# Performance work log

Measured on AMD Instinct MI355X. Metric: run time of the kernel, lower is better.

## Reference

```python
import jax, jax.numpy as jnp
import numpy as np

B, S, D = 32, 256, 384
MAX_LEN = 4096
DUR_MAX = 16  # durations in [0, 16)


def setup_inputs() -> dict:
    key = jax.random.key(0)
    kx, kd = jax.random.split(key)
    x = jax.random.normal(kx, (B, S, D), dtype=jnp.float32)
    duration = jax.random.randint(kd, (B, S), 0, DUR_MAX, dtype=jnp.int64)
    return {"x": x, "duration": duration, "max_len": MAX_LEN}


def reference(x, duration, max_len):
    # Length regulation: repeat row i of x[b] duration[b, i] times, then pad
    # each batch element with zeros to max_len frames.
    # Equivalent vectorized form: frame t of batch b copies phoneme index
    #   idx = searchsorted(cumsum(duration[b]), t, side='right')
    # and frames beyond total duration are zero.
    Bx, Sx, Dx = x.shape
    cum = jnp.cumsum(duration, axis=1)          # [B, S] cumulative frame ends
    mel_len = cum[:, -1]                        # [B] total frames per batch
    t = jnp.arange(max_len)                     # [T]
    # For each batch row, map each output frame t -> source phoneme index.
    idx = jax.vmap(lambda c: jnp.searchsorted(c, t, side='right'))(cum)  # [B, T]
    idx = jnp.clip(idx, 0, Sx - 1)
    out = jnp.take_along_axis(x, idx[:, :, None], axis=1)  # [B, T, D] gather
    mask = (t[None, :] < mel_len[:, None])                  # [B, T] valid frames
    out = out * mask[:, :, None].astype(x.dtype)            # zero-pad tail
    return out, mel_len
```

## Files before the change

kernel.cpp:

```cpp
#include <hip/hip_runtime.h>


constexpr int B  = 32;
constexpr int S  = 256;
constexpr int D  = 384;
constexpr int ML = 4096;
constexpr int D4 = D / 4;
constexpr int ROWS = 16;
constexpr int TB = 256;

__global__ __launch_bounds__(TB) void lr_scan_kernel(const int* __restrict__ dur,
                                                     int* __restrict__ cum,
                                                     float* __restrict__ mel_out) {
    const int b = blockIdx.x;
    const int tid = threadIdx.x;
    __shared__ int s[S];
    s[tid] = dur[b * S + tid];
    __syncthreads();
    for (int off = 1; off < S; off <<= 1) {
        int v = (tid >= off) ? s[tid - off] : 0;
        __syncthreads();
        s[tid] += v;
        __syncthreads();
    }
    cum[b * S + tid] = s[tid];
    if (tid == S - 1) mel_out[b] = (float)s[tid];
}

__global__ __launch_bounds__(TB) void lr_expand_kernel(const float4* __restrict__ x,
                                                       const int* __restrict__ cum,
                                                       float4* __restrict__ out) {
    constexpr int RPB = ML / ROWS;
    const int b      = blockIdx.x / RPB;
    const int rowblk = blockIdx.x % RPB;
    const int tid    = threadIdx.x;

    __shared__ int scum[S];
    __shared__ int sidx[ROWS];
    scum[tid] = cum[b * S + tid];
    __syncthreads();
    const int mel = scum[S - 1];

    if (tid < ROWS) {
        const int t = rowblk * ROWS + tid;
        int lo = 0, hi = S;
        while (lo < hi) {
            int mid = (lo + hi) >> 1;
            if (scum[mid] <= t) lo = mid + 1; else hi = mid;
        }
        sidx[tid] = (lo < S) ? lo : (S - 1);
    }
    __syncthreads();

    const float4* xb = x + (size_t)b * S * D4;
    float4* ob = out + ((size_t)b * ML + (size_t)rowblk * ROWS) * D4;

    for (int j = tid; j < ROWS * D4; j += TB) {
        const int tl = j / D4;
        const int d4 = j - tl * D4;
        const int t  = rowblk * ROWS + tl;
        float4 v;
        if (t < mel) {
            v = xb[(size_t)sidx[tl] * D4 + d4];
        } else {
            v = make_float4(0.f, 0.f, 0.f, 0.f);
        }
        ob[j] = v;
    }
}

extern "C" void kernel_launch(void* const* d_in, const int* in_sizes, int n_in,
                              void* d_out, int out_size, void* d_ws, size_t ws_size,
                              hipStream_t stream) {
    const float* x   = (const float*)d_in[0];
    const int*   dur = (const int*)d_in[1];
    float* out = (float*)d_out;
    int*   cum = (int*)d_ws;
    float* mel_out = out + (size_t)B * ML * D;

    lr_scan_kernel<<<B, TB, 0, stream>>>(dur, cum, mel_out);
    lr_expand_kernel<<<B * (ML / ROWS), TB, 0, stream>>>(
        (const float4*)x, cum, (float4*)out);
}
```

Measured before the change: 39.46 us.

## Fuse duration scan into expand kernel with wave-shuffle scan and nontemporal stores

Drops the separate scan kernel. Each expand block now recomputes the cumulative durations for its batch with a 64-lane shuffle scan plus a cross-wave fixup, which removes one launch and the global round trip through workspace. Rows per block go from 16 to 32, the copy loop is unrolled, and output stores are nontemporal to avoid polluting the cache. In exchange, every block redundantly reads and scans 256 durations.

```diff
diff --git a/kernel.cpp b/kernel.cpp
--- a/kernel.cpp
+++ b/kernel.cpp
@@ -1,71 +1,71 @@
 #include <hip/hip_runtime.h>
 
 
-constexpr int B  = 32;
-constexpr int S  = 256;
-constexpr int D  = 384;
-constexpr int ML = 4096;
-constexpr int D4 = D / 4;
-constexpr int ROWS = 16;
-constexpr int TB = 256;
+typedef float f32x4 __attribute__((ext_vector_type(4)));
 
-__global__ __launch_bounds__(TB) void lr_scan_kernel(const int* __restrict__ dur,
-                                                     int* __restrict__ cum,
-                                                     float* __restrict__ mel_out) {
-    const int b = blockIdx.x;
-    const int tid = threadIdx.x;
-    __shared__ int s[S];
-    s[tid] = dur[b * S + tid];
-    __syncthreads();
-    for (int off = 1; off < S; off <<= 1) {
-        int v = (tid >= off) ? s[tid - off] : 0;
-        __syncthreads();
-        s[tid] += v;
-        __syncthreads();
-    }
-    cum[b * S + tid] = s[tid];
-    if (tid == S - 1) mel_out[b] = (float)s[tid];
-}
+constexpr int B    = 32;
+constexpr int S    = 256;
+constexpr int D    = 384;
+constexpr int ML   = 4096;
+constexpr int D4   = D / 4;
+constexpr int ROWS = 32;
+constexpr int TB   = 256;
+constexpr int RPB  = ML / ROWS;
 
-__global__ __launch_bounds__(TB) void lr_expand_kernel(const float4* __restrict__ x,
-                                                       const int* __restrict__ cum,
-                                                       float4* __restrict__ out) {
-    constexpr int RPB = ML / ROWS;
+__global__ __launch_bounds__(TB) void lr_fused_kernel(const f32x4* __restrict__ x,
+                                                      const int*   __restrict__ dur,
+                                                      f32x4*       __restrict__ out,
+                                                      float*       __restrict__ mel_out) {
     const int b      = blockIdx.x / RPB;
     const int rowblk = blockIdx.x % RPB;
     const int tid    = threadIdx.x;
 
     __shared__ int scum[S];
+    __shared__ int wsum[TB / 64];
     __shared__ int sidx[ROWS];
-    scum[tid] = cum[b * S + tid];
+
+    int v = dur[b * S + tid];
+    #pragma unroll
+    for (int off = 1; off < 64; off <<= 1) {
+        int n = __shfl_up(v, off, 64);
+        if ((tid & 63) >= off) v += n;
+    }
+    if ((tid & 63) == 63) wsum[tid >> 6] = v;
     __syncthreads();
+    int add = 0;
+    const int w = tid >> 6;
+    #pragma unroll
+    for (int i = 0; i < TB / 64; ++i)
+        if (i < w) add += wsum[i];
+    v += add;
+    scum[tid] = v;
+    __syncthreads();
+
     const int mel = scum[S - 1];
+    if (rowblk == 0 && tid == S - 1) mel_out[b] = (float)v;
 
     if (tid < ROWS) {
         const int t = rowblk * ROWS + tid;
         int lo = 0, hi = S;
         while (lo < hi) {
-            int mid = (lo + hi) >> 1;
+            const int mid = (lo + hi) >> 1;
             if (scum[mid] <= t) lo = mid + 1; else hi = mid;
         }
         sidx[tid] = (lo < S) ? lo : (S - 1);
     }
     __syncthreads();
 
-    const float4* xb = x + (size_t)b * S * D4;
-    float4* ob = out + ((size_t)b * ML + (size_t)rowblk * ROWS) * D4;
+    const f32x4* xb = x + (size_t)b * S * D4;
+    f32x4* ob = out + ((size_t)b * ML + (size_t)rowblk * ROWS) * D4;
+    const f32x4 z = (f32x4){0.f, 0.f, 0.f, 0.f};
 
+    #pragma unroll
     for (int j = tid; j < ROWS * D4; j += TB) {
         const int tl = j / D4;
         const int d4 = j - tl * D4;
         const int t  = rowblk * ROWS + tl;
-        float4 v;
-        if (t < mel) {
-            v = xb[(size_t)sidx[tl] * D4 + d4];
-        } else {
-            v = make_float4(0.f, 0.f, 0.f, 0.f);
-        }
-        ob[j] = v;
+        f32x4 vv = (t < mel) ? xb[(size_t)sidx[tl] * D4 + d4] : z;
+        __builtin_nontemporal_store(vv, &ob[j]);
     }
 }
 
@@ -75,10 +75,8 @@
     const float* x   = (const float*)d_in[0];
     const int*   dur = (const int*)d_in[1];
     float* out = (float*)d_out;
-    int*   cum = (int*)d_ws;
     float* mel_out = out + (size_t)B * ML * D;
 
-    lr_scan_kernel<<<B, TB, 0, stream>>>(dur, cum, mel_out);
-    lr_expand_kernel<<<B * (ML / ROWS), TB, 0, stream>>>(
-        (const float4*)x, cum, (float4*)out);
+    lr_fused_kernel<<<B * RPB, TB, 0, stream>>>(
+        (const f32x4*)x, dur, (f32x4*)out, mel_out);
 }
```

Result: slower. 45.06 us (+14.2%).
